# Optimization experiments

Hardware: AMD Instinct MI355X
Metric: run time of the kernel (lower is better)

The kernel has to match this reference:

```python
import math
import jax, jax.numpy as jnp
import numpy as np

B, S, D, H = 2, 2048, 1024, 16
HD = D // H  # head_dim = 64


def setup_inputs() -> dict:
    key = jax.random.key(0)
    ks = jax.random.split(key, 5)
    scale = 1.0 / math.sqrt(D)
    return {
        "x": jax.random.normal(ks[0], (B, S, D), dtype=jnp.float32),
        "Wq": jax.random.normal(ks[1], (D, D), dtype=jnp.float32) * scale,
        "Wk": jax.random.normal(ks[2], (D, D), dtype=jnp.float32) * scale,
        "Wv": jax.random.normal(ks[3], (D, D), dtype=jnp.float32) * scale,
        "Wo": jax.random.normal(ks[4], (D, D), dtype=jnp.float32) * scale,
    }


def reference(x, Wq, Wk, Wv, Wo):
    b, s, d = x.shape
    def split_heads(t):
        return t.reshape(b, s, H, HD).swapaxes(1, 2)  # [b, H, s, HD]

    q = split_heads(x @ Wq)
    k = split_heads(x @ Wk)
    v = split_heads(x @ Wv)

    # [b, H, s, s] scores with causal mask, stable softmax
    scores = jnp.einsum("bhqd,bhkd->bhqk", q, k) / math.sqrt(HD)
    causal_mask = jnp.triu(jnp.ones((s, s), dtype=bool), k=1)
    scores = jnp.where(causal_mask, -jnp.inf, scores)
    weights = jax.nn.softmax(scores, axis=-1)

    attended = jnp.einsum("bhqk,bhkd->bhqd", weights, v)
    combined = attended.swapaxes(1, 2).reshape(b, s, d)
    return combined @ Wo
```

## Files before the change

### kernel.cpp

```cpp
#include <hip/hip_runtime.h>
#include <math.h>

#define BATCH 2
#define SEQ   2048
#define DMODEL 1024
#define NHEAD 16
#define HEADD 64
#define MROWS 4096

typedef __attribute__((ext_vector_type(8))) __bf16 bf16x8;
typedef __attribute__((ext_vector_type(4))) float f32x4;

__device__ __forceinline__ ushort f2bf(float f) {
    uint u = __float_as_uint(f);
    u += 0x7fffu + ((u >> 16) & 1u);
    return (ushort)(u >> 16);
}
__device__ __forceinline__ float bf2f(ushort h) {
    return __uint_as_float(((uint)h) << 16);
}
__device__ __forceinline__ ushort4 pack4bf(float a, float b, float c, float d) {
    union { __bf16 h[4]; ushort4 u; } p;
    p.h[0] = (__bf16)a; p.h[1] = (__bf16)b; p.h[2] = (__bf16)c; p.h[3] = (__bf16)d;
    return p.u;
}

#define GLD16(gsrc, ldst)                                                         \
    __builtin_amdgcn_global_load_lds(                                             \
        (const __attribute__((address_space(1))) unsigned int*)(gsrc),            \
        (__attribute__((address_space(3))) unsigned int*)(ldst), 16, 0, 0)

#define QSCALE 0.1803368801111204f
#define MFIX   16.0f

__global__ __launch_bounds__(256) void prep(const float* __restrict__ x,
                                            const float* __restrict__ Wq,
                                            const float* __restrict__ Wk,
                                            const float* __restrict__ Wv,
                                            const float* __restrict__ Wo,
                                            ushort* __restrict__ wtc,
                                            ushort* __restrict__ woh,
                                            ushort* __restrict__ xh) {
    const int z = blockIdx.z;
    const int t = threadIdx.x;
    if (z == 4) {
        const int n4 = MROWS * DMODEL / 4;
        int i = (blockIdx.y * 16 + blockIdx.x) * 256 + t;
        const int stride = 256 * 256;
        for (; i < n4; i += stride) {
            const float4 v = reinterpret_cast<const float4*>(x)[i];
            ushort4 h;
            h.x = f2bf(v.x); h.y = f2bf(v.y); h.z = f2bf(v.z); h.w = f2bf(v.w);
            reinterpret_cast<ushort4*>(xh)[i] = h;
        }
        return;
    }
    const float* W = (z == 0) ? Wq : (z == 1) ? Wk : (z == 2) ? Wv : Wo;
    __shared__ float T[64][68];
    const int k0 = blockIdx.y * 64, n0 = blockIdx.x * 64;
    {
        const int r = t >> 2, c0 = (t & 3) * 16;
        #pragma unroll
        for (int j = 0; j < 4; ++j)
            *reinterpret_cast<float4*>(&T[r][c0 + j * 4]) =
                *reinterpret_cast<const float4*>(&W[(size_t)(k0 + r) * DMODEL + n0 + c0 + j * 4]);
    }
    __syncthreads();
    const int nl = t >> 2, kq = t & 3;
    ushort hb[16];
    #pragma unroll
    for (int e = 0; e < 16; ++e) hb[e] = f2bf(T[kq * 16 + e][nl]);
    if (z < 3) {
        const size_t o = (size_t)(z * 1024 + n0 + nl) * DMODEL + k0 + kq * 16;
        *reinterpret_cast<uint4*>(&wtc[o]) = *reinterpret_cast<uint4*>(&hb[0]);
        *reinterpret_cast<uint4*>(&wtc[o + 8]) = *reinterpret_cast<uint4*>(&hb[8]);
    } else {
        const size_t o = (size_t)(n0 + nl) * DMODEL + k0 + kq * 16;
        *reinterpret_cast<uint4*>(&woh[o]) = *reinterpret_cast<uint4*>(&hb[0]);
        *reinterpret_cast<uint4*>(&woh[o + 8]) = *reinterpret_cast<uint4*>(&hb[8]);
    }
}

__global__ __launch_bounds__(256, 3) void gemm_qkv(const ushort* __restrict__ xh,
                                                   const ushort* __restrict__ wtc,
                                                   ushort* __restrict__ Qb,
                                                   ushort* __restrict__ Kb,
                                                   ushort* __restrict__ Vtb) {
    __shared__ ushort SH[17408];
    ushort* const Ah = SH;
    ushort* const Bh = SH + 8192;

    const int t = threadIdx.x, lane = t & 63, w = t >> 6;
    const int l = lane & 15, g = lane >> 4;
    const int wm = w >> 1, wn = w & 1;
    const int bm = blockIdx.y * 128, bn = blockIdx.x * 128;

    f32x4 acc[4][4];
    #pragma unroll
    for (int mt = 0; mt < 4; ++mt)
        #pragma unroll
        for (int nt = 0; nt < 4; ++nt) acc[mt][nt] = (f32x4){0.f, 0.f, 0.f, 0.f};

    for (int kt = 0; kt < DMODEL; kt += 64) {
        __syncthreads();
        #pragma unroll
        for (int i = 0; i < 8; ++i) {
            const int sid = w * 8 + i;
            const int c = sid & 15;
            const ushort* src = (sid < 16) ? xh : wtc;
            const int rb = (sid < 16) ? bm : bn;
            ushort* dst = ((sid < 16) ? Ah : Bh) + c * 512;
            const int row = c * 8 + (lane >> 3);
            const int sw = ((lane & 7) ^ (row & 7)) << 3;
            GLD16(src + (size_t)(rb + row) * DMODEL + kt + sw, dst);
        }
        __syncthreads();

        bf16x8 af[4][2], bf[4][2];
        #pragma unroll
        for (int mt = 0; mt < 4; ++mt)
            #pragma unroll
            for (int s = 0; s < 2; ++s) {
                const int m = wm * 64 + mt * 16 + l;
                af[mt][s] = *reinterpret_cast<const bf16x8*>(&Ah[m * 64 + (((g + 4 * s) ^ (m & 7)) << 3)]);
            }
        #pragma unroll
        for (int nt = 0; nt < 4; ++nt)
            #pragma unroll
            for (int s = 0; s < 2; ++s) {
                const int n = wn * 64 + nt * 16 + l;
                bf[nt][s] = *reinterpret_cast<const bf16x8*>(&Bh[n * 64 + (((g + 4 * s) ^ (n & 7)) << 3)]);
            }
        __builtin_amdgcn_s_setprio(1);
        #pragma unroll
        for (int mt = 0; mt < 4; ++mt)
            #pragma unroll
            for (int nt = 0; nt < 4; ++nt)
                #pragma unroll
                for (int s = 0; s < 2; ++s)
                    acc[mt][nt] = __builtin_amdgcn_mfma_f32_16x16x32_bf16(af[mt][s], bf[nt][s], acc[mt][nt], 0, 0, 0);
        __builtin_amdgcn_s_setprio(0);
    }

    const int mode = bn >> 10;
    if (mode == 0) {
        #pragma unroll
        for (int mt = 0; mt < 4; ++mt)
            #pragma unroll
            for (int nt = 0; nt < 4; ++nt)
                #pragma unroll
                for (int r = 0; r < 4; ++r) {
                    const int row = bm + wm * 64 + mt * 16 + g * 4 + r;
                    const int col = bn + wn * 64 + nt * 16 + l;
                    Qb[(size_t)row * DMODEL + col] = f2bf(acc[mt][nt][r] * QSCALE);
                }
    } else if (mode == 1) {
        #pragma unroll
        for (int mt = 0; mt < 4; ++mt)
            #pragma unroll
            for (int nt = 0; nt < 4; ++nt)
                #pragma unroll
                for (int r = 0; r < 4; ++r) {
                    const int row = bm + wm * 64 + mt * 16 + g * 4 + r;
                    const int col = (bn - 1024) + wn * 64 + nt * 16 + l;
                    Kb[(size_t)row * DMODEL + col] = f2bf(acc[mt][nt][r]);
                }
    } else {
        __syncthreads();
        ushort* VtL = SH;
        #pragma unroll
        for (int mt = 0; mt < 4; ++mt)
            #pragma unroll
            for (int nt = 0; nt < 4; ++nt)
                #pragma unroll
                for (int r = 0; r < 4; ++r) {
                    const int dl = wn * 64 + nt * 16 + l;
                    const int kl = wm * 64 + mt * 16 + g * 4 + r;
                    VtL[dl * 136 + kl] = f2bf(acc[mt][nt][r]);
                }
        __syncthreads();
        const int dl = t >> 1, kq = t & 1;
        const int b = bm >> 11;
        const int row = b * 1024 + (bn - 2048) + dl;
        const int key0 = bm & 2047;
        const size_t o = (size_t)row * SEQ + key0 + kq * 64;
        #pragma unroll
        for (int j = 0; j < 8; ++j)
            *reinterpret_cast<uint4*>(&Vtb[o + j * 8]) =
                *reinterpret_cast<uint4*>(&VtL[dl * 136 + kq * 64 + j * 8]);
    }
}

__global__ __launch_bounds__(256, 4) void attn(const ushort* __restrict__ Q,
                                               const ushort* __restrict__ K,
                                               const ushort* __restrict__ Vt,
                                               ushort* __restrict__ ATh) {
    __shared__ ushort Kl[2 * 4096];
    __shared__ ushort Vl[2 * 4096];
    __shared__ ushort Pl[4096];

    const int t = threadIdx.x, lane = t & 63, w = t >> 6;
    const int l = lane & 15, g = lane >> 4;
    const int tile = 31 - blockIdx.y;
    const int bh = blockIdx.x, b = bh >> 4, h = bh & 15;
    const size_t kbase = (size_t)b * SEQ * DMODEL + h * 64;
    const size_t vbase = (size_t)bh * 64 * SEQ;
    const int q0 = tile * 64 + w * 16;
    const int nch = tile + 1;

    union { ushort u[8]; bf16x8 v; } onesu;
    #pragma unroll
    for (int e = 0; e < 8; ++e) onesu.u[e] = 0x3F80;
    const bf16x8 ONES = onesu.v;

    bf16x8 qf[2];
    {
        const size_t qo = (size_t)(b * SEQ + q0 + l) * DMODEL + h * 64 + 8 * g;
        qf[0] = *reinterpret_cast<const bf16x8*>(&Q[qo]);
        qf[1] = *reinterpret_cast<const bf16x8*>(&Q[qo + 32]);
    }

    f32x4 accO[4];
    #pragma unroll
    for (int dt = 0; dt < 4; ++dt) accO[dt] = (f32x4){0.f, 0.f, 0.f, 0.f};
    f32x4 accL = (f32x4){0.f, 0.f, 0.f, 0.f};

    auto STAGE = [&](int buf, int kc) {
        const int k0 = kc * 64;
        if (w < 2) {
            #pragma unroll
            for (int i = 0; i < 4; ++i) {
                const int c = w * 4 + i;
                const int row = c * 8 + (lane >> 3);
                const int sw = ((lane & 7) ^ (row & 7)) << 3;
                GLD16(K + kbase + (size_t)(k0 + row) * DMODEL + sw,
                      Kl + buf * 4096 + c * 512);
            }
        } else {
            #pragma unroll
            for (int i = 0; i < 4; ++i) {
                const int c = (w - 2) * 4 + i;
                const int row = c * 8 + (lane >> 3);
                const int sw = ((lane & 7) ^ (row & 7)) << 3;
                GLD16(Vt + vbase + (size_t)row * SEQ + k0 + sw,
                      Vl + buf * 4096 + c * 512);
            }
        }
    };

    auto COMPUTE = [&](int buf, int kc) {
        const int k0 = kc * 64;
        const ushort* Kb_ = Kl + buf * 4096;
        const ushort* Vb_ = Vl + buf * 4096;
        const int xorsw0 = ((g + 0) ^ (l & 7)) << 3;
        const int xorsw1 = ((g + 4) ^ (l & 7)) << 3;

        bf16x8 kf[4][2];
        #pragma unroll
        for (int nt = 0; nt < 4; ++nt) {
            const int ro = (nt * 16 + l) * 64;
            kf[nt][0] = *reinterpret_cast<const bf16x8*>(&Kb_[ro + xorsw0]);
            kf[nt][1] = *reinterpret_cast<const bf16x8*>(&Kb_[ro + xorsw1]);
        }

        f32x4 sc[4];
        __builtin_amdgcn_s_setprio(1);
        #pragma unroll
        for (int nt = 0; nt < 4; ++nt) {
            f32x4 z = (f32x4){-MFIX, -MFIX, -MFIX, -MFIX};
            z = __builtin_amdgcn_mfma_f32_16x16x32_bf16(kf[nt][0], qf[0], z, 0, 0, 0);
            z = __builtin_amdgcn_mfma_f32_16x16x32_bf16(kf[nt][1], qf[1], z, 0, 0, 0);
            sc[nt] = z;
        }
        __builtin_amdgcn_s_setprio(0);

        if (kc == nch - 1) {
            const int qg = q0 + l;
            #pragma unroll
            for (int nt = 0; nt < 4; ++nt)
                #pragma unroll
                for (int r = 0; r < 4; ++r)
                    if (k0 + nt * 16 + g * 4 + r > qg) sc[nt][r] = -INFINITY;
        }

        {
            #pragma unroll
            for (int nt = 0; nt < 4; ++nt)
                #pragma unroll
                for (int r = 0; r < 4; ++r)
                    sc[nt][r] = exp2f(sc[nt][r]);

            const int prow = w * 16 + l;
            #pragma unroll
            for (int nt = 0; nt < 4; ++nt)
                *reinterpret_cast<ushort4*>(
                    &Pl[prow * 64 + ((nt * 16 + 4 * g) ^ ((l & 7) << 3))]) =
                    pack4bf(sc[nt][0], sc[nt][1], sc[nt][2], sc[nt][3]);
        }

        bf16x8 vf[4][2];
        #pragma unroll
        for (int dt = 0; dt < 4; ++dt) {
            const int ro = (dt * 16 + l) * 64;
            vf[dt][0] = *reinterpret_cast<const bf16x8*>(&Vb_[ro + xorsw0]);
            vf[dt][1] = *reinterpret_cast<const bf16x8*>(&Vb_[ro + xorsw1]);
        }
        bf16x8 pf[2];
        const int prow = w * 16 + l;
        pf[0] = *reinterpret_cast<const bf16x8*>(&Pl[prow * 64 + ((8 * g) ^ ((l & 7) << 3))]);
        pf[1] = *reinterpret_cast<const bf16x8*>(&Pl[prow * 64 + ((32 + 8 * g) ^ ((l & 7) << 3))]);
        __builtin_amdgcn_s_setprio(1);
        #pragma unroll
        for (int dt = 0; dt < 4; ++dt) {
            accO[dt] = __builtin_amdgcn_mfma_f32_16x16x32_bf16(pf[0], vf[dt][0], accO[dt], 0, 0, 0);
            accO[dt] = __builtin_amdgcn_mfma_f32_16x16x32_bf16(pf[1], vf[dt][1], accO[dt], 0, 0, 0);
        }
        accL = __builtin_amdgcn_mfma_f32_16x16x32_bf16(pf[0], ONES, accL, 0, 0, 0);
        accL = __builtin_amdgcn_mfma_f32_16x16x32_bf16(pf[1], ONES, accL, 0, 0, 0);
        __builtin_amdgcn_s_setprio(0);
    };

    STAGE(0, 0);
    __syncthreads();

    int cur = 0;
    for (int kc = 0; kc < nch; ++kc) {
        if (kc + 1 < nch) STAGE(cur ^ 1, kc + 1);
        COMPUTE(cur, kc);
        __syncthreads();
        cur ^= 1;
    }

    #pragma unroll
    for (int r = 0; r < 4; ++r) {
        const float inv = 1.f / accL[r];
        const size_t row = (size_t)(b * SEQ + q0 + g * 4 + r) * DMODEL + h * 64;
        #pragma unroll
        for (int dt = 0; dt < 4; ++dt)
            ATh[row + dt * 16 + l] = f2bf(accO[dt][r] * inv);
    }
}

__global__ __launch_bounds__(512) void gemm_o(const ushort* __restrict__ Ahg,
                                              const ushort* __restrict__ Bhg,
                                              float* __restrict__ C) {
    __shared__ ushort SH[12288];
    ushort* const Ah = SH;
    ushort* const Bh = SH + 8192;

    const int t = threadIdx.x, lane = t & 63, w = t >> 6;
    const int l = lane & 15, g = lane >> 4;
    const int wm = w >> 1, wn = w & 1;
    const int bm = blockIdx.y * 128, bn = blockIdx.x * 64;

    f32x4 acc[2][2];
    #pragma unroll
    for (int mt = 0; mt < 2; ++mt)
        #pragma unroll
        for (int nt = 0; nt < 2; ++nt) acc[mt][nt] = (f32x4){0.f, 0.f, 0.f, 0.f};

    for (int kt = 0; kt < DMODEL; kt += 64) {
        __syncthreads();
        #pragma unroll
        for (int i = 0; i < 3; ++i) {
            const int sid = w * 3 + i;
            const ushort* src; ushort* dst; int rb, c;
            if (sid < 16) { src = Ahg; dst = Ah; rb = bm; c = sid; }
            else          { src = Bhg; dst = Bh; rb = bn; c = sid - 16; }
            const int row = c * 8 + (lane >> 3);
            const int sw = ((lane & 7) ^ (row & 7)) << 3;
            GLD16(src + (size_t)(rb + row) * DMODEL + kt + sw, dst + c * 512);
        }
        __syncthreads();

        bf16x8 ah[2][2], bhf[2][2];
        #pragma unroll
        for (int mt = 0; mt < 2; ++mt)
            #pragma unroll
            for (int s = 0; s < 2; ++s) {
                const int m = wm * 32 + mt * 16 + l;
                ah[mt][s] = *reinterpret_cast<const bf16x8*>(&Ah[m * 64 + (((g + 4 * s) ^ (m & 7)) << 3)]);
            }
        #pragma unroll
        for (int nt = 0; nt < 2; ++nt)
            #pragma unroll
            for (int s = 0; s < 2; ++s) {
                const int n = wn * 32 + nt * 16 + l;
                bhf[nt][s] = *reinterpret_cast<const bf16x8*>(&Bh[n * 64 + (((g + 4 * s) ^ (n & 7)) << 3)]);
            }
        __builtin_amdgcn_s_setprio(1);
        #pragma unroll
        for (int mt = 0; mt < 2; ++mt)
            #pragma unroll
            for (int nt = 0; nt < 2; ++nt)
                #pragma unroll
                for (int s = 0; s < 2; ++s)
                    acc[mt][nt] = __builtin_amdgcn_mfma_f32_16x16x32_bf16(ah[mt][s], bhf[nt][s], acc[mt][nt], 0, 0, 0);
        __builtin_amdgcn_s_setprio(0);
    }

    #pragma unroll
    for (int mt = 0; mt < 2; ++mt)
        #pragma unroll
        for (int nt = 0; nt < 2; ++nt)
            #pragma unroll
            for (int r = 0; r < 4; ++r) {
                const int row = bm + wm * 32 + mt * 16 + g * 4 + r;
                const int col = bn + wn * 32 + nt * 16 + l;
                C[(size_t)row * DMODEL + col] = acc[mt][nt][r];
            }
}

extern "C" void kernel_launch(void* const* d_in, const int* in_sizes, int n_in,
                              void* d_out, int out_size, void* d_ws, size_t ws_size,
                              hipStream_t stream) {
    const float* x  = (const float*)d_in[0];
    const float* Wq = (const float*)d_in[1];
    const float* Wk = (const float*)d_in[2];
    const float* Wv = (const float*)d_in[3];
    const float* Wo = (const float*)d_in[4];
    float* out = (float*)d_out;

    char* ws = (char*)d_ws;
    const size_t MB = 1024 * 1024;
    ushort* xh  = (ushort*)(ws);
    ushort* ath = xh;
    ushort* wtc = (ushort*)(ws + 16 * MB);
    ushort* woh = (ushort*)(ws + 22 * MB);
    ushort* Qb  = (ushort*)(ws + 26 * MB);
    ushort* Kb  = (ushort*)(ws + 34 * MB);
    ushort* Vtb = (ushort*)(ws + 42 * MB);

    prep<<<dim3(16, 16, 5), 256, 0, stream>>>(x, Wq, Wk, Wv, Wo, wtc, woh, xh);

    gemm_qkv<<<dim3(24, 32), 256, 0, stream>>>(xh, wtc, Qb, Kb, Vtb);

    attn<<<dim3(32, 32), 256, 0, stream>>>(Qb, Kb, Vtb, ath);

    gemm_o<<<dim3(16, 32), 512, 0, stream>>>(ath, woh, out);
}
```

Measured before the change: 102.8 us.

## Keep softmax probabilities in registers by computing transposed PV product

The attention kernel no longer writes P to shared memory and reads it back. It computes O^T = V^T·P^T, so the score MFMA output layout can feed directly as the B operand, with V fragments gathered as pairs of 4-element loads. The output store becomes vectorized 4-wide per lane, and the launch-bounds occupancy hint rises from 4 to 5 blocks. The cost is more, smaller LDS loads for V, possible bank conflicts, and more register pressure under the tighter occupancy hint.

```diff
diff --git a/kernel.cpp b/kernel.cpp
--- a/kernel.cpp
+++ b/kernel.cpp
@@ -191,13 +191,12 @@
     }
 }
 
-__global__ __launch_bounds__(256, 4) void attn(const ushort* __restrict__ Q,
+__global__ __launch_bounds__(256, 5) void attn(const ushort* __restrict__ Q,
                                                const ushort* __restrict__ K,
                                                const ushort* __restrict__ Vt,
                                                ushort* __restrict__ ATh) {
     __shared__ ushort Kl[2 * 4096];
     __shared__ ushort Vl[2 * 4096];
-    __shared__ ushort Pl[4096];
 
     const int t = threadIdx.x, lane = t & 63, w = t >> 6;
     const int l = lane & 15, g = lane >> 4;
@@ -283,40 +282,38 @@
                     if (k0 + nt * 16 + g * 4 + r > qg) sc[nt][r] = -INFINITY;
         }
 
-        {
-            #pragma unroll
-            for (int nt = 0; nt < 4; ++nt)
-                #pragma unroll
-                for (int r = 0; r < 4; ++r)
-                    sc[nt][r] = exp2f(sc[nt][r]);
-
-            const int prow = w * 16 + l;
-            #pragma unroll
-            for (int nt = 0; nt < 4; ++nt)
-                *reinterpret_cast<ushort4*>(
-                    &Pl[prow * 64 + ((nt * 16 + 4 * g) ^ ((l & 7) << 3))]) =
-                    pack4bf(sc[nt][0], sc[nt][1], sc[nt][2], sc[nt][3]);
-        }
-
-        bf16x8 vf[4][2];
+        #pragma unroll
+        for (int nt = 0; nt < 4; ++nt)
+            #pragma unroll
+            for (int r = 0; r < 4; ++r)
+                sc[nt][r] = exp2f(sc[nt][r]);
+
+        union { ushort4 h[2]; bf16x8 v; } pb0, pb1;
+        pb0.h[0] = pack4bf(sc[0][0], sc[0][1], sc[0][2], sc[0][3]);
+        pb0.h[1] = pack4bf(sc[1][0], sc[1][1], sc[1][2], sc[1][3]);
+        pb1.h[0] = pack4bf(sc[2][0], sc[2][1], sc[2][2], sc[2][3]);
+        pb1.h[1] = pack4bf(sc[3][0], sc[3][1], sc[3][2], sc[3][3]);
+
+        const int lo = 4 * (g & 1);
+        const int bb = g >> 1;
+        const int x0 = ((0 + bb) ^ (l & 7)) << 3;
+        const int x1 = ((2 + bb) ^ (l & 7)) << 3;
+        const int x2 = ((4 + bb) ^ (l & 7)) << 3;
+        const int x3 = ((6 + bb) ^ (l & 7)) << 3;
+        __builtin_amdgcn_s_setprio(1);
         #pragma unroll
         for (int dt = 0; dt < 4; ++dt) {
-            const int ro = (dt * 16 + l) * 64;
-            vf[dt][0] = *reinterpret_cast<const bf16x8*>(&Vb_[ro + xorsw0]);
-            vf[dt][1] = *reinterpret_cast<const bf16x8*>(&Vb_[ro + xorsw1]);
-        }
-        bf16x8 pf[2];
-        const int prow = w * 16 + l;
-        pf[0] = *reinterpret_cast<const bf16x8*>(&Pl[prow * 64 + ((8 * g) ^ ((l & 7) << 3))]);
-        pf[1] = *reinterpret_cast<const bf16x8*>(&Pl[prow * 64 + ((32 + 8 * g) ^ ((l & 7) << 3))]);
-        __builtin_amdgcn_s_setprio(1);
-        #pragma unroll
-        for (int dt = 0; dt < 4; ++dt) {
-            accO[dt] = __builtin_amdgcn_mfma_f32_16x16x32_bf16(pf[0], vf[dt][0], accO[dt], 0, 0, 0);
-            accO[dt] = __builtin_amdgcn_mfma_f32_16x16x32_bf16(pf[1], vf[dt][1], accO[dt], 0, 0, 0);
-        }
-        accL = __builtin_amdgcn_mfma_f32_16x16x32_bf16(pf[0], ONES, accL, 0, 0, 0);
-        accL = __builtin_amdgcn_mfma_f32_16x16x32_bf16(pf[1], ONES, accL, 0, 0, 0);
+            const int vrow = (dt * 16 + l) * 64;
+            union { ushort4 h[2]; bf16x8 v; } va0, va1;
+            va0.h[0] = *reinterpret_cast<const ushort4*>(&Vb_[vrow + x0 + lo]);
+            va0.h[1] = *reinterpret_cast<const ushort4*>(&Vb_[vrow + x1 + lo]);
+            va1.h[0] = *reinterpret_cast<const ushort4*>(&Vb_[vrow + x2 + lo]);
+            va1.h[1] = *reinterpret_cast<const ushort4*>(&Vb_[vrow + x3 + lo]);
+            accO[dt] = __builtin_amdgcn_mfma_f32_16x16x32_bf16(va0.v, pb0.v, accO[dt], 0, 0, 0);
+            accO[dt] = __builtin_amdgcn_mfma_f32_16x16x32_bf16(va1.v, pb1.v, accO[dt], 0, 0, 0);
+        }
+        accL = __builtin_amdgcn_mfma_f32_16x16x32_bf16(ONES, pb0.v, accL, 0, 0, 0);
+        accL = __builtin_amdgcn_mfma_f32_16x16x32_bf16(ONES, pb1.v, accL, 0, 0, 0);
         __builtin_amdgcn_s_setprio(0);
     };
 
@@ -331,13 +328,15 @@
         cur ^= 1;
     }
 
-    #pragma unroll
-    for (int r = 0; r < 4; ++r) {
-        const float inv = 1.f / accL[r];
-        const size_t row = (size_t)(b * SEQ + q0 + g * 4 + r) * DMODEL + h * 64;
-        #pragma unroll
-        for (int dt = 0; dt < 4; ++dt)
-            ATh[row + dt * 16 + l] = f2bf(accO[dt][r] * inv);
+    {
+        const float inv = 1.f / accL[0];
+        const size_t row = (size_t)(b * SEQ + q0 + l) * DMODEL + h * 64;
+        #pragma unroll
+        for (int dt = 0; dt < 4; ++dt) {
+            const ushort4 o = pack4bf(accO[dt][0] * inv, accO[dt][1] * inv,
+                                      accO[dt][2] * inv, accO[dt][3] * inv);
+            *reinterpret_cast<ushort4*>(&ATh[row + dt * 16 + 4 * g]) = o;
+        }
     }
 }
 
```

After: 107.0 us. +4.1%, slower.
